# Optimization experiments

Measured on AMD Instinct MI355X. Metric: run time of the kernel, lower is better.

The kernel has to match this reference:

```python
import jax, jax.numpy as jnp
import numpy as np
import math

D_MODEL = 1024
D_STATE = 64
BATCH = 16
LENGTH = 4096


def _hippo_legs(n_dim: int) -> np.ndarray:
    """HiPPO-LegS matrix, scaled by 0.5 as in the torch module."""
    n = np.arange(n_dim)[:, None].astype(np.float32)
    k = np.arange(n_dim)[None, :].astype(np.float32)
    a = np.where(n > k, -np.sqrt(2.0 * n + 1.0) * np.sqrt(2.0 * k + 1.0), 0.0)
    a = a + np.diag(-(np.arange(n_dim, dtype=np.float32) + 1.0))
    return (a * 0.5).astype(np.float32)


def setup_inputs() -> dict:
    key = jax.random.key(0)
    k_u, k_B, k_C, k_dt = jax.random.split(key, 4)
    u = jax.random.normal(k_u, (BATCH, LENGTH, D_MODEL), dtype=jnp.float32)
    A = jnp.asarray(_hippo_legs(D_STATE))
    B = jax.random.normal(k_B, (D_STATE, D_MODEL), dtype=jnp.float32) * 0.01
    C = jax.random.normal(k_C, (D_MODEL, D_STATE), dtype=jnp.float32) * 0.01
    D = jnp.ones((D_MODEL,), dtype=jnp.float32)
    log_dt = (jax.random.uniform(k_dt, (D_MODEL,), dtype=jnp.float32)
              * (math.log(0.1) - math.log(0.001)) + math.log(0.001))
    return {"u": u, "A": A, "B": B, "C": C, "D": D, "log_dt": log_dt}


def reference(u, A, B, C, D, log_dt):
    # u: (B, L, d_model)
    d_state = A.shape[0]
    dt_mean = jnp.exp(log_dt).mean()
    a_bar = jnp.eye(d_state, dtype=u.dtype) + dt_mean * A  # (N, N)
    # Precompute input projection for every timestep: (L, B, N)
    bu = jnp.einsum('bld,nd->lbn', u, dt_mean * B)

    def step(x, bu_t):
        # x: (B, N); x_{t} = x_{t-1} @ a_bar.T + (u_t @ b_bar.T)
        x = x @ a_bar.T + bu_t
        return x, x

    x0 = jnp.zeros((u.shape[0], d_state), dtype=u.dtype)
    _, xs = jax.lax.scan(step, x0, bu)  # xs: (L, B, N)
    y = jnp.einsum('lbn,dn->bld', xs, C) + u * D  # (B, L, d_model)
    return y
```

## Files before the change

### kernel.cpp

```cpp
#include <hip/hip_runtime.h>


#define DM   1024
#define DS   64
#define NB   16
#define LL   4096
#define LC   64
#define NCH  (LL / LC)
#define MTOT (NB * LL)

#define WS_ABAR 64
#define WS_APOW (WS_ABAR + 4096)
#define WS_TMP  (WS_APOW + 4096)
#define WS_E    (WS_TMP + 4096)
#define WS_S    (WS_E + NB * NCH * DS)
#define WS_BU   (WS_S + NB * NCH * DS)

__global__ __launch_bounds__(256) void k_prep(const float* __restrict__ A,
                                              const float* __restrict__ log_dt,
                                              float* __restrict__ ws) {
    __shared__ float red[256];
    int tid = threadIdx.x;
    float s = 0.f;
    for (int i = tid; i < DM; i += 256) s += expf(log_dt[i]);
    red[tid] = s;
    __syncthreads();
    for (int off = 128; off > 0; off >>= 1) {
        if (tid < off) red[tid] += red[tid + off];
        __syncthreads();
    }
    float dt = red[0] * (1.f / (float)DM);
    if (tid == 0) ws[0] = dt;
    for (int idx = tid; idx < 4096; idx += 256) {
        int n = idx >> 6, m = idx & 63;
        ws[WS_ABAR + idx] = dt * A[idx] + ((n == m) ? 1.f : 0.f);
    }
}

__global__ __launch_bounds__(256) void k_matsq(const float* __restrict__ src,
                                               float* __restrict__ dst) {
    __shared__ float s[64][65];
    int tid = threadIdx.x;
#pragma unroll
    for (int rep = 0; rep < 16; ++rep) {
        int idx = rep * 256 + tid;
        s[idx >> 6][idx & 63] = src[idx];
    }
    __syncthreads();
    int n = (blockIdx.x << 2) + (tid >> 6);
    int m = tid & 63;
    float acc = 0.f;
#pragma unroll
    for (int k = 0; k < 64; ++k) acc = fmaf(s[n][k], s[k][m], acc);
    dst[(n << 6) + m] = acc;
}

__global__ __launch_bounds__(256) void k_gemm1(const float* __restrict__ u,
                                               const float* __restrict__ Bm,
                                               const float* __restrict__ ws,
                                               float* __restrict__ bu) {
    __shared__ float u_lds[128][68];
    __shared__ float bt_lds[64][68];
    int tid = threadIdx.x;
    int m0 = blockIdx.x * 128;
    float dt = ws[0];
    int rg = tid >> 3, c8 = tid & 7;
    float acc[4][8];
#pragma unroll
    for (int i = 0; i < 4; ++i)
#pragma unroll
        for (int j = 0; j < 8; ++j) acc[i][j] = 0.f;

    for (int kt = 0; kt < 16; ++kt) {
        int k0 = kt * 64;
#pragma unroll
        for (int rep = 0; rep < 8; ++rep) {
            int idx = rep * 256 + tid;
            int r = idx >> 4, c4 = (idx & 15) << 2;
            float4 v = *reinterpret_cast<const float4*>(&u[(size_t)(m0 + r) * DM + k0 + c4]);
            *reinterpret_cast<float4*>(&u_lds[r][c4]) = v;
        }
#pragma unroll
        for (int rep = 0; rep < 16; ++rep) {
            int idx = rep * 256 + tid;
            int n = idx >> 6, k = idx & 63;
            bt_lds[k][n] = Bm[n * DM + k0 + k];
        }
        __syncthreads();
#pragma unroll
        for (int k4 = 0; k4 < 64; k4 += 4) {
            float4 a[4];
#pragma unroll
            for (int i = 0; i < 4; ++i)
                a[i] = *reinterpret_cast<float4*>(&u_lds[rg + 32 * i][k4]);
            float4 b0[4], b1[4];
#pragma unroll
            for (int kk = 0; kk < 4; ++kk) {
                b0[kk] = *reinterpret_cast<float4*>(&bt_lds[k4 + kk][c8 * 4]);
                b1[kk] = *reinterpret_cast<float4*>(&bt_lds[k4 + kk][c8 * 4 + 32]);
            }
#pragma unroll
            for (int i = 0; i < 4; ++i) {
                float av[4] = {a[i].x, a[i].y, a[i].z, a[i].w};
#pragma unroll
                for (int kk = 0; kk < 4; ++kk) {
                    acc[i][0] = fmaf(av[kk], b0[kk].x, acc[i][0]);
                    acc[i][1] = fmaf(av[kk], b0[kk].y, acc[i][1]);
                    acc[i][2] = fmaf(av[kk], b0[kk].z, acc[i][2]);
                    acc[i][3] = fmaf(av[kk], b0[kk].w, acc[i][3]);
                    acc[i][4] = fmaf(av[kk], b1[kk].x, acc[i][4]);
                    acc[i][5] = fmaf(av[kk], b1[kk].y, acc[i][5]);
                    acc[i][6] = fmaf(av[kk], b1[kk].z, acc[i][6]);
                    acc[i][7] = fmaf(av[kk], b1[kk].w, acc[i][7]);
                }
            }
        }
        __syncthreads();
    }
#pragma unroll
    for (int i = 0; i < 4; ++i) {
        size_t row = (size_t)(m0 + rg + 32 * i);
#pragma unroll
        for (int h = 0; h < 2; ++h) {
            float4 o;
            o.x = dt * acc[i][h * 4 + 0];
            o.y = dt * acc[i][h * 4 + 1];
            o.z = dt * acc[i][h * 4 + 2];
            o.w = dt * acc[i][h * 4 + 3];
            *reinterpret_cast<float4*>(&bu[row * DS + c8 * 4 + 32 * h]) = o;
        }
    }
}

template <int PASS>
__global__ __launch_bounds__(256) void k_scan(float* __restrict__ ws) {
    const float* Abar = ws + WS_ABAR;
    float* bu = ws + WS_BU;
    int tid = threadIdx.x;
    int w = tid >> 6, lane = tid & 63;
    int task = blockIdx.x * 4 + w;
    int b = task >> 6;
    int j = task & 63;
    __shared__ float xbuf[4][64];

    float a_row[64];
#pragma unroll
    for (int mg = 0; mg < 16; ++mg) {
        float4 v = *reinterpret_cast<const float4*>(&Abar[lane * 64 + mg * 4]);
        a_row[mg * 4 + 0] = v.x; a_row[mg * 4 + 1] = v.y;
        a_row[mg * 4 + 2] = v.z; a_row[mg * 4 + 3] = v.w;
    }
    float x;
    if (PASS == 0) x = 0.f;
    else           x = ws[WS_S + (size_t)task * DS + lane];

    float* bub = bu + ((size_t)b * LL + (size_t)j * LC) * DS;
    float buv = bub[lane];
    for (int t = 0; t < LC; ++t) {
        float bunext = 0.f;
        if (t + 1 < LC) bunext = bub[(t + 1) * DS + lane];
        xbuf[w][lane] = x;
        asm volatile("" ::: "memory");
        float xn = buv;
#pragma unroll
        for (int mg = 0; mg < 16; ++mg) {
            float4 xm = *reinterpret_cast<float4*>(&xbuf[w][mg * 4]);
            xn = fmaf(a_row[mg * 4 + 0], xm.x, xn);
            xn = fmaf(a_row[mg * 4 + 1], xm.y, xn);
            xn = fmaf(a_row[mg * 4 + 2], xm.z, xn);
            xn = fmaf(a_row[mg * 4 + 3], xm.w, xn);
        }
        asm volatile("" ::: "memory");
        x = xn;
        if (PASS == 1) bub[t * DS + lane] = x;
        buv = bunext;
    }
    if (PASS == 0) ws[WS_E + (size_t)task * DS + lane] = x;
}

__global__ __launch_bounds__(64) void k_combine(float* __restrict__ ws) {
    const float* Apow = ws + WS_APOW;
    int b = blockIdx.x;
    int lane = threadIdx.x;
    __shared__ float xbuf[64];
    float p_row[64];
#pragma unroll
    for (int mg = 0; mg < 16; ++mg) {
        float4 v = *reinterpret_cast<const float4*>(&Apow[lane * 64 + mg * 4]);
        p_row[mg * 4 + 0] = v.x; p_row[mg * 4 + 1] = v.y;
        p_row[mg * 4 + 2] = v.z; p_row[mg * 4 + 3] = v.w;
    }
    float x = 0.f;
    for (int jj = 0; jj < NCH; ++jj) {
        size_t task = (size_t)b * NCH + jj;
        ws[WS_S + task * DS + lane] = x;
        float e = ws[WS_E + task * DS + lane];
        xbuf[lane] = x;
        asm volatile("" ::: "memory");
        float xn = e;
#pragma unroll
        for (int mg = 0; mg < 16; ++mg) {
            float4 xm = *reinterpret_cast<float4*>(&xbuf[mg * 4]);
            xn = fmaf(p_row[mg * 4 + 0], xm.x, xn);
            xn = fmaf(p_row[mg * 4 + 1], xm.y, xn);
            xn = fmaf(p_row[mg * 4 + 2], xm.z, xn);
            xn = fmaf(p_row[mg * 4 + 3], xm.w, xn);
        }
        asm volatile("" ::: "memory");
        x = xn;
    }
}

__global__ __launch_bounds__(256) void k_gemm2(const float* __restrict__ u,
                                               const float* __restrict__ C,
                                               const float* __restrict__ Dv,
                                               const float* __restrict__ ws,
                                               float* __restrict__ y) {
    __shared__ float xs_lds[128][68];
    __shared__ float ct_lds[64][132];
    const float* xs = ws + WS_BU;
    int tid = threadIdx.x;
    int m0 = blockIdx.x * 128;
    int d0 = blockIdx.y * 128;
#pragma unroll
    for (int rep = 0; rep < 8; ++rep) {
        int idx = rep * 256 + tid;
        int r = idx >> 4, c4 = (idx & 15) << 2;
        float4 v = *reinterpret_cast<const float4*>(&xs[(size_t)(m0 + r) * DS + c4]);
        *reinterpret_cast<float4*>(&xs_lds[r][c4]) = v;
    }
#pragma unroll
    for (int rep = 0; rep < 32; ++rep) {
        int idx = rep * 256 + tid;
        int n = idx & 63, dl = idx >> 6;
        ct_lds[n][dl] = C[(size_t)(d0 + dl) * DS + n];
    }
    __syncthreads();

    int rg = tid >> 3, c8 = tid & 7;
    float acc[4][16];
#pragma unroll
    for (int i = 0; i < 4; ++i)
#pragma unroll
        for (int j = 0; j < 16; ++j) acc[i][j] = 0.f;

#pragma unroll 4
    for (int n = 0; n < 64; ++n) {
        float xv[4];
#pragma unroll
        for (int i = 0; i < 4; ++i) xv[i] = xs_lds[rg + 32 * i][n];
        float4 cv[4];
#pragma unroll
        for (int q = 0; q < 4; ++q)
            cv[q] = *reinterpret_cast<float4*>(&ct_lds[n][c8 * 4 + 32 * q]);
#pragma unroll
        for (int i = 0; i < 4; ++i) {
#pragma unroll
            for (int q = 0; q < 4; ++q) {
                acc[i][q * 4 + 0] = fmaf(xv[i], cv[q].x, acc[i][q * 4 + 0]);
                acc[i][q * 4 + 1] = fmaf(xv[i], cv[q].y, acc[i][q * 4 + 1]);
                acc[i][q * 4 + 2] = fmaf(xv[i], cv[q].z, acc[i][q * 4 + 2]);
                acc[i][q * 4 + 3] = fmaf(xv[i], cv[q].w, acc[i][q * 4 + 3]);
            }
        }
    }
#pragma unroll
    for (int i = 0; i < 4; ++i) {
        size_t row = (size_t)(m0 + rg + 32 * i);
#pragma unroll
        for (int q = 0; q < 4; ++q) {
            int c = d0 + c8 * 4 + 32 * q;
            float4 uv = *reinterpret_cast<const float4*>(&u[row * DM + c]);
            float4 dv = *reinterpret_cast<const float4*>(&Dv[c]);
            float4 o;
            o.x = acc[i][q * 4 + 0] + uv.x * dv.x;
            o.y = acc[i][q * 4 + 1] + uv.y * dv.y;
            o.z = acc[i][q * 4 + 2] + uv.z * dv.z;
            o.w = acc[i][q * 4 + 3] + uv.w * dv.w;
            *reinterpret_cast<float4*>(&y[row * DM + c]) = o;
        }
    }
}

extern "C" void kernel_launch(void* const* d_in, const int* in_sizes, int n_in,
                              void* d_out, int out_size, void* d_ws, size_t ws_size,
                              hipStream_t stream) {
    (void)in_sizes; (void)n_in; (void)out_size; (void)ws_size;
    const float* u      = (const float*)d_in[0];
    const float* A      = (const float*)d_in[1];
    const float* Bm     = (const float*)d_in[2];
    const float* C      = (const float*)d_in[3];
    const float* Dv     = (const float*)d_in[4];
    const float* log_dt = (const float*)d_in[5];
    float* y  = (float*)d_out;
    float* ws = (float*)d_ws;
    float* bu = ws + WS_BU;

    k_prep<<<dim3(1), dim3(256), 0, stream>>>(A, log_dt, ws);
    k_matsq<<<dim3(16), dim3(256), 0, stream>>>(ws + WS_ABAR, ws + WS_TMP);
    k_matsq<<<dim3(16), dim3(256), 0, stream>>>(ws + WS_TMP,  ws + WS_APOW);
    k_matsq<<<dim3(16), dim3(256), 0, stream>>>(ws + WS_APOW, ws + WS_TMP);
    k_matsq<<<dim3(16), dim3(256), 0, stream>>>(ws + WS_TMP,  ws + WS_APOW);
    k_matsq<<<dim3(16), dim3(256), 0, stream>>>(ws + WS_APOW, ws + WS_TMP);
    k_matsq<<<dim3(16), dim3(256), 0, stream>>>(ws + WS_TMP,  ws + WS_APOW);

    k_gemm1<<<dim3(MTOT / 128), dim3(256), 0, stream>>>(u, Bm, ws, bu);
    k_scan<0><<<dim3(NB * NCH / 4), dim3(256), 0, stream>>>(ws);
    k_combine<<<dim3(NB), dim3(64), 0, stream>>>(ws);
    k_scan<1><<<dim3(NB * NCH / 4), dim3(256), 0, stream>>>(ws);
    k_gemm2<<<dim3(MTOT / 128, DM / 128), dim3(256), 0, stream>>>(u, C, Dv, ws, y);
}
```

Baseline: 392.9 us.

## Use split-bf16 MFMA for both GEMMs and fuse matrix-power prep kernels

Both projection GEMMs now use bf16 MFMA instructions with a hi/lo split (three products) to keep near-fp32 accuracy, replacing scalar FMA loops. The scan writes its states as packed bf16 hi/lo pairs so the output GEMM can load them directly, and that GEMM now uses 64-wide column tiles with an LDS-staged epilogue. The six matrix-squaring launches are folded into a single prep kernel. The scan and combine inner products are split into four partial sums to shorten the dependency chain. The split-bf16 scheme loses some precision relative to fp32 and triples the MFMA work.

Result: slower. 547.4 us (+39.3%).

```diff
diff --git a/kernel.cpp b/kernel.cpp
--- a/kernel.cpp
+++ b/kernel.cpp
@@ -11,15 +11,28 @@
 
 #define WS_ABAR 64
 #define WS_APOW (WS_ABAR + 4096)
-#define WS_TMP  (WS_APOW + 4096)
-#define WS_E    (WS_TMP + 4096)
+#define WS_E    (WS_APOW + 4096)
 #define WS_S    (WS_E + NB * NCH * DS)
 #define WS_BU   (WS_S + NB * NCH * DS)
 
-__global__ __launch_bounds__(256) void k_prep(const float* __restrict__ A,
-                                              const float* __restrict__ log_dt,
-                                              float* __restrict__ ws) {
+typedef __attribute__((ext_vector_type(4))) float f32x4;
+typedef __attribute__((ext_vector_type(8))) short bf16x8;
+
+__device__ inline unsigned short bf16_rne(float f) {
+    unsigned u = __builtin_bit_cast(unsigned, f);
+    u += 0x7FFFu + ((u >> 16) & 1u);
+    return (unsigned short)(u >> 16);
+}
+__device__ inline float bf16f(unsigned short h) {
+    unsigned u = ((unsigned)h) << 16;
+    return __builtin_bit_cast(float, u);
+}
+
+__global__ __launch_bounds__(256) void k_prep_pow(const float* __restrict__ A,
+                                                  const float* __restrict__ log_dt,
+                                                  float* __restrict__ ws) {
     __shared__ float red[256];
+    __shared__ float m0[64][65], m1[64][65];
     int tid = threadIdx.x;
     float s = 0.f;
     for (int i = tid; i < DM; i += 256) s += expf(log_dt[i]);
@@ -33,43 +46,52 @@
     if (tid == 0) ws[0] = dt;
     for (int idx = tid; idx < 4096; idx += 256) {
         int n = idx >> 6, m = idx & 63;
-        ws[WS_ABAR + idx] = dt * A[idx] + ((n == m) ? 1.f : 0.f);
-    }
-}
-
-__global__ __launch_bounds__(256) void k_matsq(const float* __restrict__ src,
-                                               float* __restrict__ dst) {
-    __shared__ float s[64][65];
-    int tid = threadIdx.x;
-#pragma unroll
-    for (int rep = 0; rep < 16; ++rep) {
-        int idx = rep * 256 + tid;
-        s[idx >> 6][idx & 63] = src[idx];
-    }
-    __syncthreads();
-    int n = (blockIdx.x << 2) + (tid >> 6);
-    int m = tid & 63;
-    float acc = 0.f;
-#pragma unroll
-    for (int k = 0; k < 64; ++k) acc = fmaf(s[n][k], s[k][m], acc);
-    dst[(n << 6) + m] = acc;
+        float v = dt * A[idx] + ((n == m) ? 1.f : 0.f);
+        m0[n][m] = v;
+        ws[WS_ABAR + idx] = v;
+    }
+    __syncthreads();
+#pragma unroll 1
+    for (int sq = 0; sq < 6; ++sq) {
+        float (*src)[65] = (sq & 1) ? m1 : m0;
+        float (*dst)[65] = (sq & 1) ? m0 : m1;
+#pragma unroll
+        for (int rep = 0; rep < 16; ++rep) {
+            int idx = rep * 256 + tid;
+            int n = idx >> 6, m = idx & 63;
+            float a0 = 0.f, a1 = 0.f, a2 = 0.f, a3 = 0.f;
+#pragma unroll
+            for (int k = 0; k < 64; k += 4) {
+                a0 = fmaf(src[n][k + 0], src[k + 0][m], a0);
+                a1 = fmaf(src[n][k + 1], src[k + 1][m], a1);
+                a2 = fmaf(src[n][k + 2], src[k + 2][m], a2);
+                a3 = fmaf(src[n][k + 3], src[k + 3][m], a3);
+            }
+            dst[n][m] = (a0 + a1) + (a2 + a3);
+        }
+        __syncthreads();
+    }
+    for (int idx = tid; idx < 4096; idx += 256)
+        ws[WS_APOW + idx] = m0[idx >> 6][idx & 63];
 }
 
 __global__ __launch_bounds__(256) void k_gemm1(const float* __restrict__ u,
                                                const float* __restrict__ Bm,
                                                const float* __restrict__ ws,
                                                float* __restrict__ bu) {
-    __shared__ float u_lds[128][68];
-    __shared__ float bt_lds[64][68];
+    __shared__ short a_hi[128][72], a_lo[128][72];
+    __shared__ short b_hi[64][72],  b_lo[64][72];
     int tid = threadIdx.x;
     int m0 = blockIdx.x * 128;
+    int wid = tid >> 6, lane = tid & 63;
+    int lr = lane & 15, lg = lane >> 4;
     float dt = ws[0];
-    int rg = tid >> 3, c8 = tid & 7;
-    float acc[4][8];
-#pragma unroll
-    for (int i = 0; i < 4; ++i)
-#pragma unroll
-        for (int j = 0; j < 8; ++j) acc[i][j] = 0.f;
+
+    f32x4 acc[2][4];
+#pragma unroll
+    for (int i = 0; i < 2; ++i)
+#pragma unroll
+        for (int j = 0; j < 4; ++j) acc[i][j] = (f32x4)(0.f);
 
     for (int kt = 0; kt < 16; ++kt) {
         int k0 = kt * 64;
@@ -78,58 +100,60 @@
             int idx = rep * 256 + tid;
             int r = idx >> 4, c4 = (idx & 15) << 2;
             float4 v = *reinterpret_cast<const float4*>(&u[(size_t)(m0 + r) * DM + k0 + c4]);
-            *reinterpret_cast<float4*>(&u_lds[r][c4]) = v;
-        }
-#pragma unroll
-        for (int rep = 0; rep < 16; ++rep) {
+            ushort4 h, l;
+            h.x = bf16_rne(v.x); l.x = bf16_rne(v.x - bf16f(h.x));
+            h.y = bf16_rne(v.y); l.y = bf16_rne(v.y - bf16f(h.y));
+            h.z = bf16_rne(v.z); l.z = bf16_rne(v.z - bf16f(h.z));
+            h.w = bf16_rne(v.w); l.w = bf16_rne(v.w - bf16f(h.w));
+            *reinterpret_cast<ushort4*>(&a_hi[r][c4]) = h;
+            *reinterpret_cast<ushort4*>(&a_lo[r][c4]) = l;
+        }
+#pragma unroll
+        for (int rep = 0; rep < 4; ++rep) {
             int idx = rep * 256 + tid;
-            int n = idx >> 6, k = idx & 63;
-            bt_lds[k][n] = Bm[n * DM + k0 + k];
+            int n = idx >> 4, k4 = (idx & 15) << 2;
+            float4 v = *reinterpret_cast<const float4*>(&Bm[(size_t)n * DM + k0 + k4]);
+            ushort4 h, l;
+            h.x = bf16_rne(v.x); l.x = bf16_rne(v.x - bf16f(h.x));
+            h.y = bf16_rne(v.y); l.y = bf16_rne(v.y - bf16f(h.y));
+            h.z = bf16_rne(v.z); l.z = bf16_rne(v.z - bf16f(h.z));
+            h.w = bf16_rne(v.w); l.w = bf16_rne(v.w - bf16f(h.w));
+            *reinterpret_cast<ushort4*>(&b_hi[n][k4]) = h;
+            *reinterpret_cast<ushort4*>(&b_lo[n][k4]) = l;
         }
         __syncthreads();
 #pragma unroll
-        for (int k4 = 0; k4 < 64; k4 += 4) {
-            float4 a[4];
-#pragma unroll
-            for (int i = 0; i < 4; ++i)
-                a[i] = *reinterpret_cast<float4*>(&u_lds[rg + 32 * i][k4]);
-            float4 b0[4], b1[4];
-#pragma unroll
-            for (int kk = 0; kk < 4; ++kk) {
-                b0[kk] = *reinterpret_cast<float4*>(&bt_lds[k4 + kk][c8 * 4]);
-                b1[kk] = *reinterpret_cast<float4*>(&bt_lds[k4 + kk][c8 * 4 + 32]);
-            }
-#pragma unroll
-            for (int i = 0; i < 4; ++i) {
-                float av[4] = {a[i].x, a[i].y, a[i].z, a[i].w};
-#pragma unroll
-                for (int kk = 0; kk < 4; ++kk) {
-                    acc[i][0] = fmaf(av[kk], b0[kk].x, acc[i][0]);
-                    acc[i][1] = fmaf(av[kk], b0[kk].y, acc[i][1]);
-                    acc[i][2] = fmaf(av[kk], b0[kk].z, acc[i][2]);
-                    acc[i][3] = fmaf(av[kk], b0[kk].w, acc[i][3]);
-                    acc[i][4] = fmaf(av[kk], b1[kk].x, acc[i][4]);
-                    acc[i][5] = fmaf(av[kk], b1[kk].y, acc[i][5]);
-                    acc[i][6] = fmaf(av[kk], b1[kk].z, acc[i][6]);
-                    acc[i][7] = fmaf(av[kk], b1[kk].w, acc[i][7]);
+        for (int kf = 0; kf < 2; ++kf) {
+            int kb = kf * 32 + lg * 8;
+            bf16x8 ah[2], al[2];
+#pragma unroll
+            for (int mf = 0; mf < 2; ++mf) {
+                ah[mf] = *reinterpret_cast<bf16x8*>(&a_hi[wid * 32 + mf * 16 + lr][kb]);
+                al[mf] = *reinterpret_cast<bf16x8*>(&a_lo[wid * 32 + mf * 16 + lr][kb]);
+            }
+#pragma unroll
+            for (int nf = 0; nf < 4; ++nf) {
+                bf16x8 bh = *reinterpret_cast<bf16x8*>(&b_hi[nf * 16 + lr][kb]);
+                bf16x8 bl = *reinterpret_cast<bf16x8*>(&b_lo[nf * 16 + lr][kb]);
+#pragma unroll
+                for (int mf = 0; mf < 2; ++mf) {
+                    acc[mf][nf] = __builtin_amdgcn_mfma_f32_16x16x32_bf16(ah[mf], bh, acc[mf][nf], 0, 0, 0);
+                    acc[mf][nf] = __builtin_amdgcn_mfma_f32_16x16x32_bf16(ah[mf], bl, acc[mf][nf], 0, 0, 0);
+                    acc[mf][nf] = __builtin_amdgcn_mfma_f32_16x16x32_bf16(al[mf], bh, acc[mf][nf], 0, 0, 0);
                 }
             }
         }
         __syncthreads();
     }
 #pragma unroll
-    for (int i = 0; i < 4; ++i) {
-        size_t row = (size_t)(m0 + rg + 32 * i);
-#pragma unroll
-        for (int h = 0; h < 2; ++h) {
-            float4 o;
-            o.x = dt * acc[i][h * 4 + 0];
-            o.y = dt * acc[i][h * 4 + 1];
-            o.z = dt * acc[i][h * 4 + 2];
-            o.w = dt * acc[i][h * 4 + 3];
-            *reinterpret_cast<float4*>(&bu[row * DS + c8 * 4 + 32 * h]) = o;
-        }
-    }
+    for (int mf = 0; mf < 2; ++mf)
+#pragma unroll
+        for (int nf = 0; nf < 4; ++nf)
+#pragma unroll
+            for (int q = 0; q < 4; ++q) {
+                size_t row = (size_t)(m0 + wid * 32 + mf * 16 + lg * 4 + q);
+                bu[row * DS + nf * 16 + lr] = dt * acc[mf][nf][q];
+            }
 }
 
 template <int PASS>
@@ -155,24 +179,34 @@
     else           x = ws[WS_S + (size_t)task * DS + lane];
 
     float* bub = bu + ((size_t)b * LL + (size_t)j * LC) * DS;
+    unsigned* bup = reinterpret_cast<unsigned*>(bub);
     float buv = bub[lane];
     for (int t = 0; t < LC; ++t) {
         float bunext = 0.f;
         if (t + 1 < LC) bunext = bub[(t + 1) * DS + lane];
         xbuf[w][lane] = x;
         asm volatile("" ::: "memory");
-        float xn = buv;
-#pragma unroll
-        for (int mg = 0; mg < 16; ++mg) {
-            float4 xm = *reinterpret_cast<float4*>(&xbuf[w][mg * 4]);
-            xn = fmaf(a_row[mg * 4 + 0], xm.x, xn);
-            xn = fmaf(a_row[mg * 4 + 1], xm.y, xn);
-            xn = fmaf(a_row[mg * 4 + 2], xm.z, xn);
-            xn = fmaf(a_row[mg * 4 + 3], xm.w, xn);
+        float part[4];
+#pragma unroll
+        for (int g = 0; g < 4; ++g) {
+            float acc = (g == 0) ? buv : 0.f;
+#pragma unroll
+            for (int q = 0; q < 4; ++q) {
+                float4 xm = *reinterpret_cast<float4*>(&xbuf[w][g * 16 + q * 4]);
+                acc = fmaf(a_row[g * 16 + q * 4 + 0], xm.x, acc);
+                acc = fmaf(a_row[g * 16 + q * 4 + 1], xm.y, acc);
+                acc = fmaf(a_row[g * 16 + q * 4 + 2], xm.z, acc);
+                acc = fmaf(a_row[g * 16 + q * 4 + 3], xm.w, acc);
+            }
+            part[g] = acc;
         }
         asm volatile("" ::: "memory");
-        x = xn;
-        if (PASS == 1) bub[t * DS + lane] = x;
+        x = (part[0] + part[1]) + (part[2] + part[3]);
+        if (PASS == 1) {
+            unsigned short h = bf16_rne(x);
+            unsigned short l = bf16_rne(x - bf16f(h));
+            bup[t * DS + lane] = (unsigned)h | ((unsigned)l << 16);
+        }
         buv = bunext;
     }
     if (PASS == 0) ws[WS_E + (size_t)task * DS + lane] = x;
@@ -197,17 +231,22 @@
         float e = ws[WS_E + task * DS + lane];
         xbuf[lane] = x;
         asm volatile("" ::: "memory");
-        float xn = e;
-#pragma unroll
-        for (int mg = 0; mg < 16; ++mg) {
-            float4 xm = *reinterpret_cast<float4*>(&xbuf[mg * 4]);
-            xn = fmaf(p_row[mg * 4 + 0], xm.x, xn);
-            xn = fmaf(p_row[mg * 4 + 1], xm.y, xn);
-            xn = fmaf(p_row[mg * 4 + 2], xm.z, xn);
-            xn = fmaf(p_row[mg * 4 + 3], xm.w, xn);
+        float part[4];
+#pragma unroll
+        for (int g = 0; g < 4; ++g) {
+            float acc = (g == 0) ? e : 0.f;
+#pragma unroll
+            for (int q = 0; q < 4; ++q) {
+                float4 xm = *reinterpret_cast<float4*>(&xbuf[g * 16 + q * 4]);
+                acc = fmaf(p_row[g * 16 + q * 4 + 0], xm.x, acc);
+                acc = fmaf(p_row[g * 16 + q * 4 + 1], xm.y, acc);
+                acc = fmaf(p_row[g * 16 + q * 4 + 2], xm.z, acc);
+                acc = fmaf(p_row[g * 16 + q * 4 + 3], xm.w, acc);
+            }
+            part[g] = acc;
         }
         asm volatile("" ::: "memory");
-        x = xn;
+        x = (part[0] + part[1]) + (part[2] + part[3]);
     }
 }
 
@@ -216,69 +255,95 @@
                                                const float* __restrict__ Dv,
                                                const float* __restrict__ ws,
                                                float* __restrict__ y) {
-    __shared__ float xs_lds[128][68];
-    __shared__ float ct_lds[64][132];
-    const float* xs = ws + WS_BU;
+    __shared__ short a_hi[128][72], a_lo[128][72];
+    __shared__ short c_hi[64][72],  c_lo[64][72];
+    const unsigned* bup = reinterpret_cast<const unsigned*>(ws + WS_BU);
     int tid = threadIdx.x;
     int m0 = blockIdx.x * 128;
-    int d0 = blockIdx.y * 128;
+    int d0 = blockIdx.y * 64;
+    int wid = tid >> 6, lane = tid & 63;
+    int lr = lane & 15, lg = lane >> 4;
+
 #pragma unroll
     for (int rep = 0; rep < 8; ++rep) {
         int idx = rep * 256 + tid;
         int r = idx >> 4, c4 = (idx & 15) << 2;
-        float4 v = *reinterpret_cast<const float4*>(&xs[(size_t)(m0 + r) * DS + c4]);
-        *reinterpret_cast<float4*>(&xs_lds[r][c4]) = v;
-    }
-#pragma unroll
-    for (int rep = 0; rep < 32; ++rep) {
+        uint4 v = *reinterpret_cast<const uint4*>(&bup[(size_t)(m0 + r) * DS + c4]);
+        ushort4 h, l;
+        h.x = (unsigned short)(v.x & 0xFFFF); l.x = (unsigned short)(v.x >> 16);
+        h.y = (unsigned short)(v.y & 0xFFFF); l.y = (unsigned short)(v.y >> 16);
+        h.z = (unsigned short)(v.z & 0xFFFF); l.z = (unsigned short)(v.z >> 16);
+        h.w = (unsigned short)(v.w & 0xFFFF); l.w = (unsigned short)(v.w >> 16);
+        *reinterpret_cast<ushort4*>(&a_hi[r][c4]) = h;
+        *reinterpret_cast<ushort4*>(&a_lo[r][c4]) = l;
+    }
+#pragma unroll
+    for (int rep = 0; rep < 4; ++rep) {
         int idx = rep * 256 + tid;
-        int n = idx & 63, dl = idx >> 6;
-        ct_lds[n][dl] = C[(size_t)(d0 + dl) * DS + n];
-    }
-    __syncthreads();
-
-    int rg = tid >> 3, c8 = tid & 7;
-    float acc[4][16];
-#pragma unroll
-    for (int i = 0; i < 4; ++i)
-#pragma unroll
-        for (int j = 0; j < 16; ++j) acc[i][j] = 0.f;
-
-#pragma unroll 4
-    for (int n = 0; n < 64; ++n) {
-        float xv[4];
-#pragma unroll
-        for (int i = 0; i < 4; ++i) xv[i] = xs_lds[rg + 32 * i][n];
-        float4 cv[4];
-#pragma unroll
-        for (int q = 0; q < 4; ++q)
-            cv[q] = *reinterpret_cast<float4*>(&ct_lds[n][c8 * 4 + 32 * q]);
-#pragma unroll
-        for (int i = 0; i < 4; ++i) {
-#pragma unroll
-            for (int q = 0; q < 4; ++q) {
-                acc[i][q * 4 + 0] = fmaf(xv[i], cv[q].x, acc[i][q * 4 + 0]);
-                acc[i][q * 4 + 1] = fmaf(xv[i], cv[q].y, acc[i][q * 4 + 1]);
-                acc[i][q * 4 + 2] = fmaf(xv[i], cv[q].z, acc[i][q * 4 + 2]);
-                acc[i][q * 4 + 3] = fmaf(xv[i], cv[q].w, acc[i][q * 4 + 3]);
-            }
-        }
-    }
-#pragma unroll
-    for (int i = 0; i < 4; ++i) {
-        size_t row = (size_t)(m0 + rg + 32 * i);
-#pragma unroll
-        for (int q = 0; q < 4; ++q) {
-            int c = d0 + c8 * 4 + 32 * q;
-            float4 uv = *reinterpret_cast<const float4*>(&u[row * DM + c]);
-            float4 dv = *reinterpret_cast<const float4*>(&Dv[c]);
-            float4 o;
-            o.x = acc[i][q * 4 + 0] + uv.x * dv.x;
-            o.y = acc[i][q * 4 + 1] + uv.y * dv.y;
-            o.z = acc[i][q * 4 + 2] + uv.z * dv.z;
-            o.w = acc[i][q * 4 + 3] + uv.w * dv.w;
-            *reinterpret_cast<float4*>(&y[row * DM + c]) = o;
-        }
+        int dl = idx >> 4, n4 = (idx & 15) << 2;
+        float4 v = *reinterpret_cast<const float4*>(&C[(size_t)(d0 + dl) * DS + n4]);
+        ushort4 h, l;
+        h.x = bf16_rne(v.x); l.x = bf16_rne(v.x - bf16f(h.x));
+        h.y = bf16_rne(v.y); l.y = bf16_rne(v.y - bf16f(h.y));
+        h.z = bf16_rne(v.z); l.z = bf16_rne(v.z - bf16f(h.z));
+        h.w = bf16_rne(v.w); l.w = bf16_rne(v.w - bf16f(h.w));
+        *reinterpret_cast<ushort4*>(&c_hi[dl][n4]) = h;
+        *reinterpret_cast<ushort4*>(&c_lo[dl][n4]) = l;
+    }
+    __syncthreads();
+
+    f32x4 acc[2][4];
+#pragma unroll
+    for (int i = 0; i < 2; ++i)
+#pragma unroll
+        for (int j = 0; j < 4; ++j) acc[i][j] = (f32x4)(0.f);
+
+#pragma unroll
+    for (int kf = 0; kf < 2; ++kf) {
+        int kb = kf * 32 + lg * 8;
+        bf16x8 ah[2], al[2];
+#pragma unroll
+        for (int mf = 0; mf < 2; ++mf) {
+            ah[mf] = *reinterpret_cast<bf16x8*>(&a_hi[wid * 32 + mf * 16 + lr][kb]);
+            al[mf] = *reinterpret_cast<bf16x8*>(&a_lo[wid * 32 + mf * 16 + lr][kb]);
+        }
+#pragma unroll
+        for (int nf = 0; nf < 4; ++nf) {
+            bf16x8 bh = *reinterpret_cast<bf16x8*>(&c_hi[nf * 16 + lr][kb]);
+            bf16x8 bl = *reinterpret_cast<bf16x8*>(&c_lo[nf * 16 + lr][kb]);
+#pragma unroll
+            for (int mf = 0; mf < 2; ++mf) {
+                acc[mf][nf] = __builtin_amdgcn_mfma_f32_16x16x32_bf16(ah[mf], bh, acc[mf][nf], 0, 0, 0);
+                acc[mf][nf] = __builtin_amdgcn_mfma_f32_16x16x32_bf16(ah[mf], bl, acc[mf][nf], 0, 0, 0);
+                acc[mf][nf] = __builtin_amdgcn_mfma_f32_16x16x32_bf16(al[mf], bh, acc[mf][nf], 0, 0, 0);
+            }
+        }
+    }
+    __syncthreads();
+    float* out_lds = reinterpret_cast<float*>(&a_hi[0][0]);
+#pragma unroll
+    for (int mf = 0; mf < 2; ++mf)
+#pragma unroll
+        for (int nf = 0; nf < 4; ++nf)
+#pragma unroll
+            for (int q = 0; q < 4; ++q)
+                out_lds[(wid * 32 + mf * 16 + lg * 4 + q) * 68 + nf * 16 + lr] = acc[mf][nf][q];
+    __syncthreads();
+#pragma unroll
+    for (int rep = 0; rep < 8; ++rep) {
+        int idx = rep * 256 + tid;
+        int r = idx >> 4, c4 = (idx & 15) << 2;
+        float4 a = *reinterpret_cast<float4*>(&out_lds[r * 68 + c4]);
+        size_t row = (size_t)(m0 + r);
+        int c = d0 + c4;
+        float4 uv = *reinterpret_cast<const float4*>(&u[row * DM + c]);
+        float4 dv = *reinterpret_cast<const float4*>(&Dv[c]);
+        float4 o;
+        o.x = a.x + uv.x * dv.x;
+        o.y = a.y + uv.y * dv.y;
+        o.z = a.z + uv.z * dv.z;
+        o.w = a.w + uv.w * dv.w;
+        *reinterpret_cast<float4*>(&y[row * DM + c]) = o;
     }
 }
 
@@ -296,17 +361,10 @@
     float* ws = (float*)d_ws;
     float* bu = ws + WS_BU;
 
-    k_prep<<<dim3(1), dim3(256), 0, stream>>>(A, log_dt, ws);
-    k_matsq<<<dim3(16), dim3(256), 0, stream>>>(ws + WS_ABAR, ws + WS_TMP);
-    k_matsq<<<dim3(16), dim3(256), 0, stream>>>(ws + WS_TMP,  ws + WS_APOW);
-    k_matsq<<<dim3(16), dim3(256), 0, stream>>>(ws + WS_APOW, ws + WS_TMP);
-    k_matsq<<<dim3(16), dim3(256), 0, stream>>>(ws + WS_TMP,  ws + WS_APOW);
-    k_matsq<<<dim3(16), dim3(256), 0, stream>>>(ws + WS_APOW, ws + WS_TMP);
-    k_matsq<<<dim3(16), dim3(256), 0, stream>>>(ws + WS_TMP,  ws + WS_APOW);
-
+    k_prep_pow<<<dim3(1), dim3(256), 0, stream>>>(A, log_dt, ws);
     k_gemm1<<<dim3(MTOT / 128), dim3(256), 0, stream>>>(u, Bm, ws, bu);
     k_scan<0><<<dim3(NB * NCH / 4), dim3(256), 0, stream>>>(ws);
     k_combine<<<dim3(NB), dim3(64), 0, stream>>>(ws);
     k_scan<1><<<dim3(NB * NCH / 4), dim3(256), 0, stream>>>(ws);
-    k_gemm2<<<dim3(MTOT / 128, DM / 128), dim3(256), 0, stream>>>(u, C, Dv, ws, y);
-}
+    k_gemm2<<<dim3(MTOT / 128, DM / 64), dim3(256), 0, stream>>>(u, C, Dv, ws, y);
+}
```
